# Kernel tuning notes

Hardware: AMD Instinct MI355X
Metric: run time of the kernel (lower is better)

Reference implementation:

```python
import jax, jax.numpy as jnp
import numpy as np

N = 100000      # nodes
E = 1600000     # edges (no self-loops; self-loops added in reference, per PyG defaults)
IN = 128        # in_size
HID = 32        # hide_size (per-head channels)
HEADS = 4       # n_heads
OUT = 128       # out_size
NEG_SLOPE = 0.2 # PyG GATConv default negative_slope


def setup_inputs() -> dict:
    key = jax.random.key(0)
    ks = jax.random.split(key, 8)
    x = jax.random.normal(ks[0], (N, IN), jnp.float32)
    # edges guaranteed non-self-loop: dst = (src + offset) % N with offset in [1, N)
    src = jax.random.randint(ks[1], (E,), 0, N, dtype=jnp.int32)
    off = jax.random.randint(ks[2], (E,), 1, N, dtype=jnp.int32)
    dst = ((src + off) % N).astype(jnp.int32)
    edge_index = jnp.stack([src, dst])  # [2, E]
    edge_weight = jax.random.uniform(ks[3], (E,), jnp.float32)
    glorot = lambda k, shape, fan: jax.random.normal(k, shape, jnp.float32) / np.sqrt(fan).astype(np.float32)
    W_gat = glorot(ks[4], (IN, HEADS * HID), IN)      # GATConv lin weight (bias=False)
    att_src = glorot(ks[5], (HEADS, HID), HID)        # GATConv att_src
    att_dst = glorot(ks[6], (HEADS, HID), HID)        # GATConv att_dst
    W_gcn = glorot(ks[7], (HEADS * HID, OUT), HEADS * HID)  # GCNConv weight (bias=False)
    return {"x": x, "edge_index": edge_index, "edge_weight": edge_weight,
            "W_gat": W_gat, "att_src": att_src, "att_dst": att_dst, "W_gcn": W_gcn}


def reference(x, edge_index, edge_weight, W_gat, att_src, att_dst, W_gcn):
    n = x.shape[0]
    loop = jnp.arange(n, dtype=edge_index.dtype)
    src = jnp.concatenate([edge_index[0], loop])  # add self-loops (PyG default)
    dst = jnp.concatenate([edge_index[1], loop])

    # ---- GATConv (concat heads, bias=False) ----
    xp = (x @ W_gat).reshape(n, HEADS, HID)                  # [N,H,C]
    a_s = jnp.einsum('nhc,hc->nh', xp, att_src)              # [N,H]
    a_d = jnp.einsum('nhc,hc->nh', xp, att_dst)
    alpha = jax.nn.leaky_relu(a_s[src] + a_d[dst], NEG_SLOPE)  # [E+N,H]
    m = jax.ops.segment_max(alpha, dst, num_segments=n)     # segment softmax over incoming edges
    e = jnp.exp(alpha - m[dst])
    denom = jax.ops.segment_sum(e, dst, num_segments=n)
    a = e / denom[dst]                                       # [E+N,H]
    y_gat = jax.ops.segment_sum(xp[src] * a[:, :, None], dst, num_segments=n)
    y_gat = y_gat.reshape(n, HEADS * HID)                    # [N, H*C]

    # ---- GCNConv (normalize=True, bias=False), self-loop weight = 1 ----
    ew = jnp.concatenate([edge_weight, jnp.ones((n,), edge_weight.dtype)])
    deg = jax.ops.segment_sum(ew, dst, num_segments=n)
    dinv = jnp.where(deg > 0, jax.lax.rsqrt(deg), 0.0)
    norm = dinv[src] * ew * dinv[dst]                        # [E+N]
    h = y_gat @ W_gcn                                        # [N, OUT]
    out = jax.ops.segment_sum(h[src] * norm[:, None], dst, num_segments=n)
    return out
```

## Files before the change

### kernel.cpp

```cpp
#include <hip/hip_runtime.h>

#define NN 100000
#define EE 1600000
#define TOT (EE + NN)
#define NEG 0.2f
#define NB 256
#define CH 391
#define TILE 4096
#define NTILES ((EE + TILE - 1) / TILE)
#define GAT_BLKS (NN / 32)
#define GEMM1_BLKS (NN / 32)
#define LDA 132

typedef unsigned int uint;
typedef unsigned short ushort;

#define BLO(u) __uint_as_float((u) << 16)
#define BHI(u) __uint_as_float((u) & 0xffff0000u)

__device__ inline ushort f2bf(float f) {
    uint u = __float_as_uint(f);
    return (ushort)((u + 0x7fff + ((u >> 16) & 1)) >> 16);
}

__device__ inline int imin(int a, int b) { return a < b ? a : b; }


__launch_bounds__(256) __global__
void k_bcount(const int* __restrict__ dst, int* __restrict__ bcnt) {
    __shared__ int h[NB];
    int t = threadIdx.x;
    h[t] = 0;
    __syncthreads();
    int base = blockIdx.x * TILE;
#pragma unroll
    for (int r = 0; r < 16; ++r) {
        int e = base + r * 256 + t;
        if (e < EE) atomicAdd(&h[dst[e] / CH], 1);
    }
    __syncthreads();
    if (h[t]) atomicAdd(&bcnt[t], h[t]);
}


__launch_bounds__(NB) __global__
void k_bprefix(const int* __restrict__ bcnt, int* __restrict__ boff,
               int* __restrict__ bcsr, int* __restrict__ bfill) {
    __shared__ int s1[NB], s2[NB];
    int t = threadIdx.x;
    int c = bcnt[t];
    int nb0 = t * CH;
    int nib = imin(nb0 + CH, NN) - nb0;
    s1[t] = c; s2[t] = c + nib;
    __syncthreads();
    for (int off = 1; off < NB; off <<= 1) {
        int a = (t >= off) ? s1[t - off] : 0;
        int b = (t >= off) ? s2[t - off] : 0;
        __syncthreads();
        s1[t] += a; s2[t] += b;
        __syncthreads();
    }
    int ex = s1[t] - c;
    boff[t] = ex;
    bfill[t] = ex;
    bcsr[t] = s2[t] - (c + nib);
    if (t == NB - 1) boff[NB] = EE;
}


__launch_bounds__(256) __global__
void k_bin(const int* __restrict__ src, const int* __restrict__ dst,
           const float* __restrict__ ew, int* __restrict__ bfill,
           long long* __restrict__ binned) {
    __shared__ long long recs[TILE];
    __shared__ ushort    bkt[TILE];
    __shared__ int hist[NB], eoff[NB], gbase[NB];
    int t = threadIdx.x;
    hist[t] = 0;
    __syncthreads();
    int base = blockIdx.x * TILE;
    int cnt = imin(TILE, EE - base);
    long long rec[16]; int binfo[16];
#pragma unroll
    for (int r = 0; r < 16; ++r) {
        int i = r * 256 + t;
        if (i < cnt) {
            int e = base + i;
            int s = src[e], d = dst[e];
            float w = ew[e];
            int b = d / CH;
            int ldst = d - b * CH;
            int rk = atomicAdd(&hist[b], 1);
            rec[r] = (long long)(uint)(s | (ldst << 17)) |
                     ((long long)__float_as_uint(w) << 32);
            binfo[r] = b | (rk << 8);
        }
    }
    __syncthreads();
    int c = hist[t];
    eoff[t] = c;
    __syncthreads();
    for (int off = 1; off < NB; off <<= 1) {
        int a = (t >= off) ? eoff[t - off] : 0;
        __syncthreads();
        eoff[t] += a;
        __syncthreads();
    }
    int ex = eoff[t] - c;
    gbase[t] = atomicAdd(&bfill[t], c);
    eoff[t] = ex;
    __syncthreads();
#pragma unroll
    for (int r = 0; r < 16; ++r) {
        int i = r * 256 + t;
        if (i < cnt) {
            int b = binfo[r] & 255, rk = binfo[r] >> 8;
            int slot = eoff[b] + rk;
            recs[slot] = rec[r];
            bkt[slot] = (ushort)b;
        }
    }
    __syncthreads();
#pragma unroll
    for (int r = 0; r < 16; ++r) {
        int i = r * 256 + t;
        if (i < cnt) {
            int b = bkt[i];
            binned[gbase[b] + (i - eoff[b])] = recs[i];
        }
    }
}


__device__ __forceinline__ void gemm1_body(
    int bid, const float* __restrict__ A, const float* __restrict__ W,
    ushort* __restrict__ C16, const float* __restrict__ att_s,
    const float* __restrict__ att_d, float* __restrict__ a_s,
    float* __restrict__ a_d, float* __restrict__ At) {
    int t = threadIdx.x;
    int lane = t & 63, wv = t >> 6;
    int rbase = bid * 32;
    const float4* Ag = (const float4*)(A + (size_t)rbase * 128);
    float4* At4 = (float4*)At;
#pragma unroll
    for (int i = 0; i < 4; ++i) At4[i * 256 + t] = Ag[i * 256 + t];
    __syncthreads();
    int r0 = wv * 8;
    int c0 = lane * 2;
    const float* wp = W + c0;
    float acc[8][2];
#pragma unroll
    for (int r = 0; r < 8; ++r) { acc[r][0] = 0.f; acc[r][1] = 0.f; }
    for (int k = 0; k < 128; k += 4) {
        float2 w0 = *(const float2*)(wp + (k + 0) * 128);
        float2 w1 = *(const float2*)(wp + (k + 1) * 128);
        float2 w2 = *(const float2*)(wp + (k + 2) * 128);
        float2 w3 = *(const float2*)(wp + (k + 3) * 128);
#pragma unroll
        for (int r = 0; r < 8; ++r) {
            float4 av = *(const float4*)(At + (r0 + r) * 128 + k);
            acc[r][0] = fmaf(av.w, w3.x, fmaf(av.z, w2.x, fmaf(av.y, w1.x, fmaf(av.x, w0.x, acc[r][0]))));
            acc[r][1] = fmaf(av.w, w3.y, fmaf(av.z, w2.y, fmaf(av.y, w1.y, fmaf(av.x, w0.y, acc[r][1]))));
        }
    }
    float as0 = att_s[c0], as1 = att_s[c0 + 1];
    float ad0 = att_d[c0], ad1 = att_d[c0 + 1];
    int head = lane >> 4;
#pragma unroll
    for (int r = 0; r < 8; ++r) {
        int row = rbase + r0 + r;
        uint pv = (uint)f2bf(acc[r][0]) | ((uint)f2bf(acc[r][1]) << 16);
        *(uint*)(C16 + (size_t)row * 128 + c0) = pv;
        float s0 = fmaf(acc[r][1], as1, acc[r][0] * as0);
        float s1 = fmaf(acc[r][1], ad1, acc[r][0] * ad0);
        s0 += __shfl_xor(s0, 1); s0 += __shfl_xor(s0, 2);
        s0 += __shfl_xor(s0, 4); s0 += __shfl_xor(s0, 8);
        s1 += __shfl_xor(s1, 1); s1 += __shfl_xor(s1, 2);
        s1 += __shfl_xor(s1, 4); s1 += __shfl_xor(s1, 8);
        if ((lane & 15) == 0) {
            a_s[row * 4 + head] = s0;
            a_d[row * 4 + head] = s1;
        }
    }
}


__launch_bounds__(256) __global__
void k_fine_gemm(const long long* __restrict__ binned, const int* __restrict__ boff,
                 const int* __restrict__ bcsr, int* __restrict__ row_off,
                 long long* __restrict__ csr,
                 const float* __restrict__ A, const float* __restrict__ W,
                 ushort* __restrict__ C16, const float* __restrict__ att_s,
                 const float* __restrict__ att_d, float* __restrict__ a_s,
                 float* __restrict__ a_d) {
    __shared__ int smem[4096];
    if (blockIdx.x >= NB) {
        gemm1_body(blockIdx.x - NB, A, W, C16, att_s, att_d, a_s, a_d,
                   (float*)smem);
        return;
    }
    int* hist = smem;
    int* excl = smem + 400;
    int* sc   = smem + 800;
    int t = threadIdx.x;
    int b = blockIdx.x;
    int e0 = boff[b], e1 = boff[b + 1];
    int nb0 = b * CH;
    int nnode = imin(CH, NN - nb0);
    const int2* __restrict__ bn = (const int2*)binned;
    hist[t] = 0;
    if (t + 256 < CH) hist[t + 256] = 0;
    __syncthreads();
    for (int i = e0 + t; i < e1; i += 256)
        atomicAdd(&hist[bn[i].x >> 17], 1);
    __syncthreads();
    int v0 = (t < nnode) ? hist[t] + 1 : 0;
    int v1 = (t + 256 < nnode) ? hist[t + 256] + 1 : 0;
    sc[t] = v0; sc[t + 256] = v1;
    __syncthreads();
    for (int off = 1; off < 512; off <<= 1) {
        int a0 = (t >= off) ? sc[t - off] : 0;
        int a1 = (t + 256 >= off) ? sc[t + 256 - off] : 0;
        __syncthreads();
        sc[t] += a0; sc[t + 256] += a1;
        __syncthreads();
    }
    int csr0 = bcsr[b];
    if (t < nnode) {
        excl[t] = csr0 + sc[t] - v0;
        row_off[nb0 + t] = excl[t];
    }
    if (t + 256 < nnode) {
        excl[t + 256] = csr0 + sc[t + 256] - v1;
        row_off[nb0 + t + 256] = excl[t + 256];
    }
    if (b == 0 && t == 0) row_off[NN] = TOT;
    hist[t] = 0;
    if (t + 256 < CH) hist[t + 256] = 0;
    __syncthreads();
    for (int i = e0 + t; i < e1; i += 256) {
        int2 r = bn[i];
        int ld = r.x >> 17;
        int rk = atomicAdd(&hist[ld], 1);
        long long rec = (long long)(uint)(r.x & 0x1FFFF) |
                        ((long long)(uint)r.y << 32);
        csr[excl[ld] + rk] = rec;
    }
    __syncthreads();
    for (int i = t; i < nnode; i += 256) {
        int n = nb0 + i;
        csr[excl[i] + hist[i]] = (long long)(uint)n | (0x3F800000LL << 32);
    }
}


__launch_bounds__(256) __global__
void k_gat_g2(const int* __restrict__ row_off, const int2* __restrict__ csr,
              const float* __restrict__ a_s, const float* __restrict__ a_d,
              const ushort* __restrict__ xp16, const float* __restrict__ W,
              ushort* __restrict__ h16, float* __restrict__ dinv) {
    __shared__ float As[32 * LDA];
    __shared__ float sdinv[32];
    int lane = threadIdx.x & 63;
    int wv = threadIdx.x >> 6;
    int grp = lane >> 4, sl = lane & 15, h2 = sl >> 2;
    int nbase = blockIdx.x * 32;

    for (int rnd = 0; rnd < 8; ++rnd) {
        int r = (rnd << 2) | wv;
        int node = nbase + r;
        int base = row_off[node], end = row_off[node + 1];
        float adh = a_d[node * 4 + h2];
        float acc[8];
#pragma unroll
        for (int j = 0; j < 8; ++j) acc[j] = 0.f;
        float den = 0.f, wsum = 0.f;
        int na = end - 1;
        int i0 = base + grp;
        int2 e0v = csr[imin(i0,      na)];
        int2 e1v = csr[imin(i0 + 4,  na)];
        int2 e2v = csr[imin(i0 + 8,  na)];
        int2 e3v = csr[imin(i0 + 12, na)];
        for (int i = i0; i < end; i += 16) {
            int2 p0 = csr[imin(i + 16, na)];
            int2 p1 = csr[imin(i + 20, na)];
            int2 p2 = csr[imin(i + 24, na)];
            int2 p3 = csr[imin(i + 28, na)];
            uint4 q0 = *(const uint4*)(xp16 + (size_t)e0v.x * 128 + sl * 8);
            uint4 q1 = *(const uint4*)(xp16 + (size_t)e1v.x * 128 + sl * 8);
            uint4 q2 = *(const uint4*)(xp16 + (size_t)e2v.x * 128 + sl * 8);
            uint4 q3 = *(const uint4*)(xp16 + (size_t)e3v.x * 128 + sl * 8);
            float al0 = a_s[e0v.x * 4 + h2] + adh;
            float al1 = a_s[e1v.x * 4 + h2] + adh;
            float al2 = a_s[e2v.x * 4 + h2] + adh;
            float al3 = a_s[e3v.x * 4 + h2] + adh;
            al0 = al0 > 0.f ? al0 : NEG * al0;
            al1 = al1 > 0.f ? al1 : NEG * al1;
            al2 = al2 > 0.f ? al2 : NEG * al2;
            al3 = al3 > 0.f ? al3 : NEG * al3;
            float aw0 = __expf(al0);
            float aw1 = (i + 4  < end) ? __expf(al1) : 0.f;
            float aw2 = (i + 8  < end) ? __expf(al2) : 0.f;
            float aw3 = (i + 12 < end) ? __expf(al3) : 0.f;
            float w0 = __int_as_float(e0v.y);
            float w1 = (i + 4  < end) ? __int_as_float(e1v.y) : 0.f;
            float w2 = (i + 8  < end) ? __int_as_float(e2v.y) : 0.f;
            float w3 = (i + 12 < end) ? __int_as_float(e3v.y) : 0.f;
            den  += (aw0 + aw1) + (aw2 + aw3);
            wsum += (w0 + w1) + (w2 + w3);
            acc[0] = fmaf(aw0, BLO(q0.x), fmaf(aw1, BLO(q1.x), fmaf(aw2, BLO(q2.x), fmaf(aw3, BLO(q3.x), acc[0]))));
            acc[1] = fmaf(aw0, BHI(q0.x), fmaf(aw1, BHI(q1.x), fmaf(aw2, BHI(q2.x), fmaf(aw3, BHI(q3.x), acc[1]))));
            acc[2] = fmaf(aw0, BLO(q0.y), fmaf(aw1, BLO(q1.y), fmaf(aw2, BLO(q2.y), fmaf(aw3, BLO(q3.y), acc[2]))));
            acc[3] = fmaf(aw0, BHI(q0.y), fmaf(aw1, BHI(q1.y), fmaf(aw2, BHI(q2.y), fmaf(aw3, BHI(q3.y), acc[3]))));
            acc[4] = fmaf(aw0, BLO(q0.z), fmaf(aw1, BLO(q1.z), fmaf(aw2, BLO(q2.z), fmaf(aw3, BLO(q3.z), acc[4]))));
            acc[5] = fmaf(aw0, BHI(q0.z), fmaf(aw1, BHI(q1.z), fmaf(aw2, BHI(q2.z), fmaf(aw3, BHI(q3.z), acc[5]))));
            acc[6] = fmaf(aw0, BLO(q0.w), fmaf(aw1, BLO(q1.w), fmaf(aw2, BLO(q2.w), fmaf(aw3, BLO(q3.w), acc[6]))));
            acc[7] = fmaf(aw0, BHI(q0.w), fmaf(aw1, BHI(q1.w), fmaf(aw2, BHI(q2.w), fmaf(aw3, BHI(q3.w), acc[7]))));
            e0v = p0; e1v = p1; e2v = p2; e3v = p3;
        }
#pragma unroll
        for (int j = 0; j < 8; ++j) {
            acc[j] += __shfl_xor(acc[j], 16);
            acc[j] += __shfl_xor(acc[j], 32);
        }
        den  += __shfl_xor(den, 16);   den  += __shfl_xor(den, 32);
        wsum += __shfl_xor(wsum, 16);  wsum += __shfl_xor(wsum, 32);
        if (grp == 0) {
            float il = 1.f / den;
            float* o = &As[r * LDA + sl * 8];
            *(float4*)(o)     = make_float4(acc[0]*il, acc[1]*il, acc[2]*il, acc[3]*il);
            *(float4*)(o + 4) = make_float4(acc[4]*il, acc[5]*il, acc[6]*il, acc[7]*il);
            if (sl == 0) {
                float dv = rsqrtf(wsum);
                sdinv[r] = dv;
                dinv[node] = dv;
            }
        }
    }
    __syncthreads();

    int r0 = wv * 8;
    int c0 = lane * 2;
    const float* __restrict__ wp = W + c0;
    float acc2[8][2];
#pragma unroll
    for (int r = 0; r < 8; ++r) { acc2[r][0] = 0.f; acc2[r][1] = 0.f; }
    for (int k = 0; k < 128; k += 4) {
        float2 w0 = *(const float2*)(wp + (k + 0) * 128);
        float2 w1 = *(const float2*)(wp + (k + 1) * 128);
        float2 w2 = *(const float2*)(wp + (k + 2) * 128);
        float2 w3 = *(const float2*)(wp + (k + 3) * 128);
#pragma unroll
        for (int r = 0; r < 8; ++r) {
            float4 av = *(const float4*)(&As[(r0 + r) * LDA + k]);
            acc2[r][0] = fmaf(av.w, w3.x, fmaf(av.z, w2.x, fmaf(av.y, w1.x, fmaf(av.x, w0.x, acc2[r][0]))));
            acc2[r][1] = fmaf(av.w, w3.y, fmaf(av.z, w2.y, fmaf(av.y, w1.y, fmaf(av.x, w0.y, acc2[r][1]))));
        }
    }
#pragma unroll
    for (int r = 0; r < 8; ++r) {
        int row = nbase + r0 + r;
        float sc2 = sdinv[r0 + r];
        uint pv = (uint)f2bf(acc2[r][0] * sc2) |
                  ((uint)f2bf(acc2[r][1] * sc2) << 16);
        *(uint*)(h16 + (size_t)row * 128 + c0) = pv;
    }
}


__launch_bounds__(256) __global__
void k_gcn(const int* __restrict__ row_off, const int2* __restrict__ csr,
           const float* __restrict__ dinv, const ushort* __restrict__ h16,
           float* __restrict__ out) {
    int lane = threadIdx.x & 63;
    int node = blockIdx.x * 4 + (threadIdx.x >> 6);
    int base = row_off[node], end = row_off[node + 1];
    float dn = dinv[node];
    int grp = lane >> 4, sl = lane & 15;
    float acc[8];
#pragma unroll
    for (int j = 0; j < 8; ++j) acc[j] = 0.f;
    int na = end - 1;
    int i0 = base + grp;
    int2 e0v = csr[imin(i0,      na)];
    int2 e1v = csr[imin(i0 + 4,  na)];
    int2 e2v = csr[imin(i0 + 8,  na)];
    int2 e3v = csr[imin(i0 + 12, na)];
    for (int i = i0; i < end; i += 16) {
        int2 p0 = csr[imin(i + 16, na)];
        int2 p1 = csr[imin(i + 20, na)];
        int2 p2 = csr[imin(i + 24, na)];
        int2 p3 = csr[imin(i + 28, na)];
        uint4 q0 = *(const uint4*)(h16 + (size_t)e0v.x * 128 + sl * 8);
        uint4 q1 = *(const uint4*)(h16 + (size_t)e1v.x * 128 + sl * 8);
        uint4 q2 = *(const uint4*)(h16 + (size_t)e2v.x * 128 + sl * 8);
        uint4 q3 = *(const uint4*)(h16 + (size_t)e3v.x * 128 + sl * 8);
        float c0 = __int_as_float(e0v.y) * dn;
        float c1 = (i + 4  < end) ? __int_as_float(e1v.y) * dn : 0.f;
        float c2 = (i + 8  < end) ? __int_as_float(e2v.y) * dn : 0.f;
        float c3 = (i + 12 < end) ? __int_as_float(e3v.y) * dn : 0.f;
        acc[0] = fmaf(c0, BLO(q0.x), fmaf(c1, BLO(q1.x), fmaf(c2, BLO(q2.x), fmaf(c3, BLO(q3.x), acc[0]))));
        acc[1] = fmaf(c0, BHI(q0.x), fmaf(c1, BHI(q1.x), fmaf(c2, BHI(q2.x), fmaf(c3, BHI(q3.x), acc[1]))));
        acc[2] = fmaf(c0, BLO(q0.y), fmaf(c1, BLO(q1.y), fmaf(c2, BLO(q2.y), fmaf(c3, BLO(q3.y), acc[2]))));
        acc[3] = fmaf(c0, BHI(q0.y), fmaf(c1, BHI(q1.y), fmaf(c2, BHI(q2.y), fmaf(c3, BHI(q3.y), acc[3]))));
        acc[4] = fmaf(c0, BLO(q0.z), fmaf(c1, BLO(q1.z), fmaf(c2, BLO(q2.z), fmaf(c3, BLO(q3.z), acc[4]))));
        acc[5] = fmaf(c0, BHI(q0.z), fmaf(c1, BHI(q1.z), fmaf(c2, BHI(q2.z), fmaf(c3, BHI(q3.z), acc[5]))));
        acc[6] = fmaf(c0, BLO(q0.w), fmaf(c1, BLO(q1.w), fmaf(c2, BLO(q2.w), fmaf(c3, BLO(q3.w), acc[6]))));
        acc[7] = fmaf(c0, BHI(q0.w), fmaf(c1, BHI(q1.w), fmaf(c2, BHI(q2.w), fmaf(c3, BHI(q3.w), acc[7]))));
        e0v = p0; e1v = p1; e2v = p2; e3v = p3;
    }
#pragma unroll
    for (int j = 0; j < 8; ++j) {
        acc[j] += __shfl_xor(acc[j], 16);
        acc[j] += __shfl_xor(acc[j], 32);
    }
    if (grp == 0) {
        float* o = out + (size_t)node * 128 + sl * 8;
        *(float4*)(o)     = make_float4(acc[0], acc[1], acc[2], acc[3]);
        *(float4*)(o + 4) = make_float4(acc[4], acc[5], acc[6], acc[7]);
    }
}


extern "C" void kernel_launch(void* const* d_in, const int* in_sizes, int n_in,
                              void* d_out, int out_size, void* d_ws, size_t ws_size,
                              hipStream_t stream) {
    const float* x    = (const float*)d_in[0];
    const int*   ei   = (const int*)  d_in[1];
    const float* ew   = (const float*)d_in[2];
    const float* Wg   = (const float*)d_in[3];
    const float* atts = (const float*)d_in[4];
    const float* attd = (const float*)d_in[5];
    const float* Wc   = (const float*)d_in[6];
    float* out = (float*)d_out;

    float* a_s   = (float*)d_ws;
    float* a_d   = a_s + 400000;
    float* dinvp = a_d + 400000;
    int* row_off = (int*)(dinvp + 100000);
    int* bcnt    = row_off + 100004;
    int* boff    = bcnt + NB;
    int* bcsr    = boff + NB + 1;
    int* bfill   = bcsr + NB;
    long long* csr = (long long*)(bfill + NB + 1);
    ushort* xp16 = (ushort*)(csr + 1700000);
    ushort* h16  = xp16 + 12800000;
    long long* binned = (long long*)h16;

    const int* srcv = ei;
    const int* dstv = ei + EE;

    hipMemsetAsync(bcnt, 0, NB * sizeof(int), stream);
    k_bcount <<<NTILES, 256, 0, stream>>>(dstv, bcnt);
    k_bprefix<<<1, NB, 0, stream>>>(bcnt, boff, bcsr, bfill);
    k_bin    <<<NTILES, 256, 0, stream>>>(srcv, dstv, ew, bfill, binned);
    k_fine_gemm<<<NB + GEMM1_BLKS, 256, 0, stream>>>(
        binned, boff, bcsr, row_off, csr,
        x, Wg, xp16, atts, attd, a_s, a_d);
    k_gat_g2<<<GAT_BLKS, 256, 0, stream>>>(row_off, (const int2*)csr, a_s, a_d,
                                           xp16, Wc, h16, dinvp);
    k_gcn  <<<NN / 4, 256, 0, stream>>>(row_off, (const int2*)csr, dinvp, h16, out);
}
```

Measured before the change: 451.3 us.

## Split fused GAT aggregation and GCN GEMM into separate kernels

The fused GAT-aggregation-plus-GEMM kernel is split into two kernels. A one-node-per-wave GAT aggregation launches 25000 blocks and writes fp32 y_gat to a new workspace buffer. A separate tiled GEMM kernel then loads 32-row tiles into shared memory and applies W_gcn with the dinv scale. This aims to remove the 8-round serial loop per block and the load imbalance from waves waiting at the barrier, which should improve latency hiding for the irregular gather. The cost is an extra 51 MB fp32 round trip through global memory and one more kernel launch.

Result: slower. 473.8 us (+5.0%).

```diff
diff --git a/kernel.cpp b/kernel.cpp
--- a/kernel.cpp
+++ b/kernel.cpp
@@ -8,9 +8,9 @@
 #define CH 391
 #define TILE 4096
 #define NTILES ((EE + TILE - 1) / TILE)
-#define GAT_BLKS (NN / 32)
+#define GAT_BLKS (NN / 4)
 #define GEMM1_BLKS (NN / 32)
-#define LDA 132
+#define GEMM2_BLKS (NN / 32)
 
 typedef unsigned int uint;
 typedef unsigned short ushort;
@@ -255,96 +255,97 @@
 
 
 __launch_bounds__(256) __global__
-void k_gat_g2(const int* __restrict__ row_off, const int2* __restrict__ csr,
-              const float* __restrict__ a_s, const float* __restrict__ a_d,
-              const ushort* __restrict__ xp16, const float* __restrict__ W,
-              ushort* __restrict__ h16, float* __restrict__ dinv) {
-    __shared__ float As[32 * LDA];
-    __shared__ float sdinv[32];
+void k_gat(const int* __restrict__ row_off, const int2* __restrict__ csr,
+           const float* __restrict__ a_s, const float* __restrict__ a_d,
+           const ushort* __restrict__ xp16,
+           float* __restrict__ ygat, float* __restrict__ dinv) {
     int lane = threadIdx.x & 63;
-    int wv = threadIdx.x >> 6;
+    int node = blockIdx.x * 4 + (threadIdx.x >> 6);
     int grp = lane >> 4, sl = lane & 15, h2 = sl >> 2;
-    int nbase = blockIdx.x * 32;
-
-    for (int rnd = 0; rnd < 8; ++rnd) {
-        int r = (rnd << 2) | wv;
-        int node = nbase + r;
-        int base = row_off[node], end = row_off[node + 1];
-        float adh = a_d[node * 4 + h2];
-        float acc[8];
-#pragma unroll
-        for (int j = 0; j < 8; ++j) acc[j] = 0.f;
-        float den = 0.f, wsum = 0.f;
-        int na = end - 1;
-        int i0 = base + grp;
-        int2 e0v = csr[imin(i0,      na)];
-        int2 e1v = csr[imin(i0 + 4,  na)];
-        int2 e2v = csr[imin(i0 + 8,  na)];
-        int2 e3v = csr[imin(i0 + 12, na)];
-        for (int i = i0; i < end; i += 16) {
-            int2 p0 = csr[imin(i + 16, na)];
-            int2 p1 = csr[imin(i + 20, na)];
-            int2 p2 = csr[imin(i + 24, na)];
-            int2 p3 = csr[imin(i + 28, na)];
-            uint4 q0 = *(const uint4*)(xp16 + (size_t)e0v.x * 128 + sl * 8);
-            uint4 q1 = *(const uint4*)(xp16 + (size_t)e1v.x * 128 + sl * 8);
-            uint4 q2 = *(const uint4*)(xp16 + (size_t)e2v.x * 128 + sl * 8);
-            uint4 q3 = *(const uint4*)(xp16 + (size_t)e3v.x * 128 + sl * 8);
-            float al0 = a_s[e0v.x * 4 + h2] + adh;
-            float al1 = a_s[e1v.x * 4 + h2] + adh;
-            float al2 = a_s[e2v.x * 4 + h2] + adh;
-            float al3 = a_s[e3v.x * 4 + h2] + adh;
-            al0 = al0 > 0.f ? al0 : NEG * al0;
-            al1 = al1 > 0.f ? al1 : NEG * al1;
-            al2 = al2 > 0.f ? al2 : NEG * al2;
-            al3 = al3 > 0.f ? al3 : NEG * al3;
-            float aw0 = __expf(al0);
-            float aw1 = (i + 4  < end) ? __expf(al1) : 0.f;
-            float aw2 = (i + 8  < end) ? __expf(al2) : 0.f;
-            float aw3 = (i + 12 < end) ? __expf(al3) : 0.f;
-            float w0 = __int_as_float(e0v.y);
-            float w1 = (i + 4  < end) ? __int_as_float(e1v.y) : 0.f;
-            float w2 = (i + 8  < end) ? __int_as_float(e2v.y) : 0.f;
-            float w3 = (i + 12 < end) ? __int_as_float(e3v.y) : 0.f;
-            den  += (aw0 + aw1) + (aw2 + aw3);
-            wsum += (w0 + w1) + (w2 + w3);
-            acc[0] = fmaf(aw0, BLO(q0.x), fmaf(aw1, BLO(q1.x), fmaf(aw2, BLO(q2.x), fmaf(aw3, BLO(q3.x), acc[0]))));
-            acc[1] = fmaf(aw0, BHI(q0.x), fmaf(aw1, BHI(q1.x), fmaf(aw2, BHI(q2.x), fmaf(aw3, BHI(q3.x), acc[1]))));
-            acc[2] = fmaf(aw0, BLO(q0.y), fmaf(aw1, BLO(q1.y), fmaf(aw2, BLO(q2.y), fmaf(aw3, BLO(q3.y), acc[2]))));
-            acc[3] = fmaf(aw0, BHI(q0.y), fmaf(aw1, BHI(q1.y), fmaf(aw2, BHI(q2.y), fmaf(aw3, BHI(q3.y), acc[3]))));
-            acc[4] = fmaf(aw0, BLO(q0.z), fmaf(aw1, BLO(q1.z), fmaf(aw2, BLO(q2.z), fmaf(aw3, BLO(q3.z), acc[4]))));
-            acc[5] = fmaf(aw0, BHI(q0.z), fmaf(aw1, BHI(q1.z), fmaf(aw2, BHI(q2.z), fmaf(aw3, BHI(q3.z), acc[5]))));
-            acc[6] = fmaf(aw0, BLO(q0.w), fmaf(aw1, BLO(q1.w), fmaf(aw2, BLO(q2.w), fmaf(aw3, BLO(q3.w), acc[6]))));
-            acc[7] = fmaf(aw0, BHI(q0.w), fmaf(aw1, BHI(q1.w), fmaf(aw2, BHI(q2.w), fmaf(aw3, BHI(q3.w), acc[7]))));
-            e0v = p0; e1v = p1; e2v = p2; e3v = p3;
-        }
-#pragma unroll
-        for (int j = 0; j < 8; ++j) {
-            acc[j] += __shfl_xor(acc[j], 16);
-            acc[j] += __shfl_xor(acc[j], 32);
-        }
-        den  += __shfl_xor(den, 16);   den  += __shfl_xor(den, 32);
-        wsum += __shfl_xor(wsum, 16);  wsum += __shfl_xor(wsum, 32);
-        if (grp == 0) {
-            float il = 1.f / den;
-            float* o = &As[r * LDA + sl * 8];
-            *(float4*)(o)     = make_float4(acc[0]*il, acc[1]*il, acc[2]*il, acc[3]*il);
-            *(float4*)(o + 4) = make_float4(acc[4]*il, acc[5]*il, acc[6]*il, acc[7]*il);
-            if (sl == 0) {
-                float dv = rsqrtf(wsum);
-                sdinv[r] = dv;
-                dinv[node] = dv;
-            }
-        }
-    }
-    __syncthreads();
-
+    int base = row_off[node], end = row_off[node + 1];
+    float adh = a_d[node * 4 + h2];
+    float acc[8];
+#pragma unroll
+    for (int j = 0; j < 8; ++j) acc[j] = 0.f;
+    float den = 0.f, wsum = 0.f;
+    int na = end - 1;
+    int i0 = base + grp;
+    int2 e0v = csr[imin(i0,      na)];
+    int2 e1v = csr[imin(i0 + 4,  na)];
+    int2 e2v = csr[imin(i0 + 8,  na)];
+    int2 e3v = csr[imin(i0 + 12, na)];
+    for (int i = i0; i < end; i += 16) {
+        int2 p0 = csr[imin(i + 16, na)];
+        int2 p1 = csr[imin(i + 20, na)];
+        int2 p2 = csr[imin(i + 24, na)];
+        int2 p3 = csr[imin(i + 28, na)];
+        uint4 q0 = *(const uint4*)(xp16 + (size_t)e0v.x * 128 + sl * 8);
+        uint4 q1 = *(const uint4*)(xp16 + (size_t)e1v.x * 128 + sl * 8);
+        uint4 q2 = *(const uint4*)(xp16 + (size_t)e2v.x * 128 + sl * 8);
+        uint4 q3 = *(const uint4*)(xp16 + (size_t)e3v.x * 128 + sl * 8);
+        float al0 = a_s[e0v.x * 4 + h2] + adh;
+        float al1 = a_s[e1v.x * 4 + h2] + adh;
+        float al2 = a_s[e2v.x * 4 + h2] + adh;
+        float al3 = a_s[e3v.x * 4 + h2] + adh;
+        al0 = al0 > 0.f ? al0 : NEG * al0;
+        al1 = al1 > 0.f ? al1 : NEG * al1;
+        al2 = al2 > 0.f ? al2 : NEG * al2;
+        al3 = al3 > 0.f ? al3 : NEG * al3;
+        float aw0 = __expf(al0);
+        float aw1 = (i + 4  < end) ? __expf(al1) : 0.f;
+        float aw2 = (i + 8  < end) ? __expf(al2) : 0.f;
+        float aw3 = (i + 12 < end) ? __expf(al3) : 0.f;
+        float w0 = __int_as_float(e0v.y);
+        float w1 = (i + 4  < end) ? __int_as_float(e1v.y) : 0.f;
+        float w2 = (i + 8  < end) ? __int_as_float(e2v.y) : 0.f;
+        float w3 = (i + 12 < end) ? __int_as_float(e3v.y) : 0.f;
+        den  += (aw0 + aw1) + (aw2 + aw3);
+        wsum += (w0 + w1) + (w2 + w3);
+        acc[0] = fmaf(aw0, BLO(q0.x), fmaf(aw1, BLO(q1.x), fmaf(aw2, BLO(q2.x), fmaf(aw3, BLO(q3.x), acc[0]))));
+        acc[1] = fmaf(aw0, BHI(q0.x), fmaf(aw1, BHI(q1.x), fmaf(aw2, BHI(q2.x), fmaf(aw3, BHI(q3.x), acc[1]))));
+        acc[2] = fmaf(aw0, BLO(q0.y), fmaf(aw1, BLO(q1.y), fmaf(aw2, BLO(q2.y), fmaf(aw3, BLO(q3.y), acc[2]))));
+        acc[3] = fmaf(aw0, BHI(q0.y), fmaf(aw1, BHI(q1.y), fmaf(aw2, BHI(q2.y), fmaf(aw3, BHI(q3.y), acc[3]))));
+        acc[4] = fmaf(aw0, BLO(q0.z), fmaf(aw1, BLO(q1.z), fmaf(aw2, BLO(q2.z), fmaf(aw3, BLO(q3.z), acc[4]))));
+        acc[5] = fmaf(aw0, BHI(q0.z), fmaf(aw1, BHI(q1.z), fmaf(aw2, BHI(q2.z), fmaf(aw3, BHI(q3.z), acc[5]))));
+        acc[6] = fmaf(aw0, BLO(q0.w), fmaf(aw1, BLO(q1.w), fmaf(aw2, BLO(q2.w), fmaf(aw3, BLO(q3.w), acc[6]))));
+        acc[7] = fmaf(aw0, BHI(q0.w), fmaf(aw1, BHI(q1.w), fmaf(aw2, BHI(q2.w), fmaf(aw3, BHI(q3.w), acc[7]))));
+        e0v = p0; e1v = p1; e2v = p2; e3v = p3;
+    }
+#pragma unroll
+    for (int j = 0; j < 8; ++j) {
+        acc[j] += __shfl_xor(acc[j], 16);
+        acc[j] += __shfl_xor(acc[j], 32);
+    }
+    den  += __shfl_xor(den, 16);   den  += __shfl_xor(den, 32);
+    wsum += __shfl_xor(wsum, 16);  wsum += __shfl_xor(wsum, 32);
+    if (grp == 0) {
+        float il = 1.f / den;
+        float* o = ygat + (size_t)node * 128 + sl * 8;
+        *(float4*)(o)     = make_float4(acc[0]*il, acc[1]*il, acc[2]*il, acc[3]*il);
+        *(float4*)(o + 4) = make_float4(acc[4]*il, acc[5]*il, acc[6]*il, acc[7]*il);
+        if (sl == 0) dinv[node] = rsqrtf(wsum);
+    }
+}
+
+
+__launch_bounds__(256) __global__
+void k_gemm2(const float* __restrict__ A, const float* __restrict__ W,
+             const float* __restrict__ dscale, ushort* __restrict__ h16) {
+    __shared__ float At[32 * 128];
+    int t = threadIdx.x;
+    int lane = t & 63, wv = t >> 6;
+    int rbase = blockIdx.x * 32;
+    const float4* Ag = (const float4*)(A + (size_t)rbase * 128);
+    float4* At4 = (float4*)At;
+#pragma unroll
+    for (int i = 0; i < 4; ++i) At4[i * 256 + t] = Ag[i * 256 + t];
+    __syncthreads();
     int r0 = wv * 8;
     int c0 = lane * 2;
-    const float* __restrict__ wp = W + c0;
-    float acc2[8][2];
-#pragma unroll
-    for (int r = 0; r < 8; ++r) { acc2[r][0] = 0.f; acc2[r][1] = 0.f; }
+    const float* wp = W + c0;
+    float acc[8][2];
+#pragma unroll
+    for (int r = 0; r < 8; ++r) { acc[r][0] = 0.f; acc[r][1] = 0.f; }
     for (int k = 0; k < 128; k += 4) {
         float2 w0 = *(const float2*)(wp + (k + 0) * 128);
         float2 w1 = *(const float2*)(wp + (k + 1) * 128);
@@ -352,17 +353,17 @@
         float2 w3 = *(const float2*)(wp + (k + 3) * 128);
 #pragma unroll
         for (int r = 0; r < 8; ++r) {
-            float4 av = *(const float4*)(&As[(r0 + r) * LDA + k]);
-            acc2[r][0] = fmaf(av.w, w3.x, fmaf(av.z, w2.x, fmaf(av.y, w1.x, fmaf(av.x, w0.x, acc2[r][0]))));
-            acc2[r][1] = fmaf(av.w, w3.y, fmaf(av.z, w2.y, fmaf(av.y, w1.y, fmaf(av.x, w0.y, acc2[r][1]))));
+            float4 av = *(const float4*)(At + (r0 + r) * 128 + k);
+            acc[r][0] = fmaf(av.w, w3.x, fmaf(av.z, w2.x, fmaf(av.y, w1.x, fmaf(av.x, w0.x, acc[r][0]))));
+            acc[r][1] = fmaf(av.w, w3.y, fmaf(av.z, w2.y, fmaf(av.y, w1.y, fmaf(av.x, w0.y, acc[r][1]))));
         }
     }
 #pragma unroll
     for (int r = 0; r < 8; ++r) {
-        int row = nbase + r0 + r;
-        float sc2 = sdinv[r0 + r];
-        uint pv = (uint)f2bf(acc2[r][0] * sc2) |
-                  ((uint)f2bf(acc2[r][1] * sc2) << 16);
+        int row = rbase + r0 + r;
+        float sc = dscale[row];
+        uint pv = (uint)f2bf(acc[r][0] * sc) |
+                  ((uint)f2bf(acc[r][1] * sc) << 16);
         *(uint*)(h16 + (size_t)row * 128 + c0) = pv;
     }
 }
@@ -434,7 +435,8 @@
     const float* Wc   = (const float*)d_in[6];
     float* out = (float*)d_out;
 
-    float* a_s   = (float*)d_ws;
+    float* ygat  = (float*)d_ws;
+    float* a_s   = ygat + 12800000;
     float* a_d   = a_s + 400000;
     float* dinvp = a_d + 400000;
     int* row_off = (int*)(dinvp + 100000);
@@ -457,7 +459,8 @@
     k_fine_gemm<<<NB + GEMM1_BLKS, 256, 0, stream>>>(
         binned, boff, bcsr, row_off, csr,
         x, Wg, xp16, atts, attd, a_s, a_d);
-    k_gat_g2<<<GAT_BLKS, 256, 0, stream>>>(row_off, (const int2*)csr, a_s, a_d,
-                                           xp16, Wc, h16, dinvp);
+    k_gat  <<<GAT_BLKS, 256, 0, stream>>>(row_off, (const int2*)csr, a_s, a_d,
+                                          xp16, ygat, dinvp);
+    k_gemm2<<<GEMM2_BLKS, 256, 0, stream>>>(ygat, Wc, dinvp, h16);
     k_gcn  <<<NN / 4, 256, 0, stream>>>(row_off, (const int2*)csr, dinvp, h16, out);
 }
```
